# Kernel tuning notes

Hardware: AMD Instinct MI355X
Metric: run time of the kernel (lower is better)

## Reference

```python
import jax, jax.numpy as jnp
import numpy as np

N_NODES = 100000
N_EDGES = 1600000
F_IN = 35
F_OUT = 5
K = 3
HID = 100


def setup_inputs() -> dict:
    key = jax.random.key(0)
    ks = jax.random.split(key, 20)
    p = lambda k, shape: (jax.random.normal(k, shape, dtype=jnp.float32) * 0.1)
    inp = {
        "x": jax.random.normal(ks[0], (N_NODES, F_IN), dtype=jnp.float32),
        "edge_index": jax.random.randint(ks[1], (2, N_EDGES), 0, N_NODES, dtype=jnp.int64),
        "edge_weight": jax.random.uniform(ks[2], (N_EDGES,), dtype=jnp.float32),
        # MLP warm-start: Linear(35,100) -> ReLU -> Linear(100,5)
        "W1": p(ks[3], (F_IN, HID)), "b1": p(ks[4], (HID,)),
        "W2": p(ks[5], (HID, F_OUT)), "b2": p(ks[6], (F_OUT,)),
        # DCRNN gates: DConv weights [2 directions, K, in+out, out]
        "Wz": p(ks[7], (2, K, F_IN + F_OUT, F_OUT)), "bz": p(ks[8], (F_OUT,)),
        "Wr": p(ks[9], (2, K, F_IN + F_OUT, F_OUT)), "br": p(ks[10], (F_OUT,)),
        "Wh": p(ks[11], (2, K, F_IN + F_OUT, F_OUT)), "bh": p(ks[12], (F_OUT,)),
        # head Linear(5,1)
        "Wl": p(ks[13], (F_OUT, 1)), "bl": p(ks[14], (1,)),
    }
    return inp


def reference(x, edge_index, edge_weight, W1, b1, W2, b2, Wz, bz, Wr, br, Wh, bh, Wl, bl):
    n = x.shape[0]
    src, dst = edge_index[0], edge_index[1]
    eps = jnp.asarray(1e-12, x.dtype)
    # random-walk normalization: forward (out-degree) and backward (in-degree) diffusion
    deg_out = jax.ops.segment_sum(edge_weight, src, num_segments=n)
    deg_in = jax.ops.segment_sum(edge_weight, dst, num_segments=n)
    w_fwd = edge_weight / jnp.maximum(deg_out[src], eps)  # [E]
    w_bwd = edge_weight / jnp.maximum(deg_in[dst], eps)   # [E]

    def prop_fwd(X):  # aggregate src -> dst
        return jax.ops.segment_sum(X[src] * w_fwd[:, None], dst, num_segments=n)

    def prop_bwd(X):  # aggregate dst -> src (reversed edges)
        return jax.ops.segment_sum(X[dst] * w_bwd[:, None], src, num_segments=n)

    def dconv(X, W, b):  # W: [2, K, Cin, Cout]
        k_steps = W.shape[1]
        out = X @ W[0, 0] + X @ W[1, 0]
        if k_steps > 1:
            Tf0, Tb0 = X, X
            Tf1, Tb1 = prop_fwd(X), prop_bwd(X)
            out = out + Tf1 @ W[0, 1] + Tb1 @ W[1, 1]
            for k in range(2, k_steps):
                Tf2 = 2.0 * prop_fwd(Tf1) - Tf0
                Tb2 = 2.0 * prop_bwd(Tb1) - Tb0
                out = out + Tf2 @ W[0, k] + Tb2 @ W[1, k]
                Tf0, Tf1 = Tf1, Tf2
                Tb0, Tb1 = Tb1, Tb2
        return out + b

    # MLP warm-start hidden state
    h1 = jax.nn.relu(x @ W1 + b1) @ W2 + b2  # [N, F_OUT]

    # DCRNN GRU cell
    XH = jnp.concatenate([x, h1], axis=1)           # [N, F_IN+F_OUT]
    Z = jax.nn.sigmoid(dconv(XH, Wz, bz))
    R = jax.nn.sigmoid(dconv(XH, Wr, br))
    XHr = jnp.concatenate([x, h1 * R], axis=1)
    H_tilde = jnp.tanh(dconv(XHr, Wh, bh))
    H = Z * h1 + (1.0 - Z) * H_tilde                # [N, F_OUT]

    y = jax.nn.relu(H) @ Wl + bl                    # [N, 1]
    A = w_fwd                                        # normalized adjacency weights [E]
    return y, A
```

## Files before the change

### kernel.cpp

```cpp
#include <hip/hip_runtime.h>
#include <hip/hip_fp16.h>

#define F_IN 35
#define F_OUT 5
#define HID 100
#define BSH 8
#define BMSK 255
#define MAXB 512

__device__ __forceinline__ unsigned qenc(float w) {
  unsigned b = __float_as_uint(w);
  int e = 127 - (int)((b >> 23) & 0xFF);
  unsigned m = (b >> 12) & 0x7FFu;
  if (e < 0) { e = 0; m = 0; }
  if (e > 15) { e = 15; m = 0; }
  return ((unsigned)e << 11) | m;
}
__device__ __forceinline__ float qdec(unsigned q) {
  return __uint_as_float(((127u - (q >> 11)) << 23) | ((q & 0x7FFu) << 12));
}

__device__ __forceinline__ float2 uph2(unsigned u) {
  __half2 h = *reinterpret_cast<const __half2*>(&u);
  return __half22float2(h);
}
__device__ __forceinline__ unsigned pkh2(float a, float b) {
  __half2 h = __floats2half2_rn(a, b);
  return *reinterpret_cast<const unsigned*>(&h);
}

__device__ __forceinline__ int ntli(const int* p) {
  return __builtin_nontemporal_load(p);
}
__device__ __forceinline__ float ntlf(const float* p) {
  return __builtin_nontemporal_load(p);
}
__device__ __forceinline__ void ntsf(float* p, float v) {
  __builtin_nontemporal_store(v, p);
}

__global__ __launch_bounds__(256) void prep_weights(
    const float* __restrict__ Wz, const float* __restrict__ Wr,
    const float* __restrict__ Wh,
    float* __restrict__ WpackA, float* __restrict__ WpackC) {
  int t = blockIdx.x * blockDim.x + threadIdx.x;
  if (t < 40 * 50) {
    int i = t / 50, c = t % 50;
    auto W = [&](const float* Wp, int d, int k, int o) {
      return Wp[((d * 3 + k) * 40 + i) * 5 + o];
    };
    float v;
    if (c < 5)       v = W(Wz,0,0,c)    + W(Wz,1,0,c)    - W(Wz,0,2,c)    - W(Wz,1,2,c);
    else if (c < 10) v = W(Wr,0,0,c-5)  + W(Wr,1,0,c-5)  - W(Wr,0,2,c-5)  - W(Wr,1,2,c-5);
    else if (c < 15) v = W(Wz,0,1,c-10);
    else if (c < 20) v = W(Wr,0,1,c-15);
    else if (c < 25) v = W(Wz,0,2,c-20);
    else if (c < 30) v = W(Wr,0,2,c-25);
    else if (c < 35) v = W(Wz,1,1,c-30);
    else if (c < 40) v = W(Wr,1,1,c-35);
    else if (c < 45) v = W(Wz,1,2,c-40);
    else             v = W(Wr,1,2,c-45);
    WpackA[i * 50 + c] = v;
  }
  if (t < 40 * 25) {
    int i = t / 25, c = t % 25;
    auto W = [&](const float* Wp, int d, int k, int o) {
      return Wp[((d * 3 + k) * 40 + i) * 5 + o];
    };
    float v;
    if (c < 5)       v = W(Wh,0,0,c)    + W(Wh,1,0,c)    - W(Wh,0,2,c)    - W(Wh,1,2,c);
    else if (c < 10) v = W(Wh,0,1,c-5);
    else if (c < 15) v = W(Wh,0,2,c-10);
    else if (c < 20) v = W(Wh,1,1,c-15);
    else             v = W(Wh,1,2,c-20);
    WpackC[i * 25 + c] = v;
  }
}

__global__ __launch_bounds__(256) void hist_kernel(
    const int* __restrict__ ei, int* __restrict__ bcnt_f,
    int* __restrict__ bcnt_b, int E) {
  __shared__ int h[2 * MAXB];
  for (int j = threadIdx.x; j < 2 * MAXB; j += blockDim.x) h[j] = 0;
  __syncthreads();
  for (int e = blockIdx.x * blockDim.x + threadIdx.x; e < E;
       e += gridDim.x * blockDim.x) {
    int s = ntli(ei + e), d = ntli(ei + E + e);
    atomicAdd(&h[d >> BSH], 1);
    atomicAdd(&h[MAXB + (s >> BSH)], 1);
  }
  __syncthreads();
  for (int j = threadIdx.x; j < 2 * MAXB; j += blockDim.x) {
    int v = h[j];
    if (v) {
      if (j < MAXB) atomicAdd(&bcnt_f[j], v);
      else          atomicAdd(&bcnt_b[j - MAXB], v);
    }
  }
}

__global__ __launch_bounds__(512) void scanb_kernel(
    const int* __restrict__ bcnt_f, const int* __restrict__ bcnt_b,
    int* __restrict__ bbase_f, int* __restrict__ bbase_b,
    int* __restrict__ bcur_f, int* __restrict__ bcur_b,
    int* __restrict__ rs_f, int* __restrict__ rs_b,
    int nbuck, int N, int E) {
  __shared__ int s0[MAXB], s1[MAXB];
  int t = threadIdx.x;
  s0[t] = (t < nbuck) ? bcnt_f[t] : 0;
  s1[t] = (t < nbuck) ? bcnt_b[t] : 0;
  __syncthreads();
  for (int off = 1; off < MAXB; off <<= 1) {
    int a = (t >= off) ? s0[t - off] : 0;
    int b = (t >= off) ? s1[t - off] : 0;
    __syncthreads();
    s0[t] += a; s1[t] += b;
    __syncthreads();
  }
  bbase_f[t + 1] = s0[t];
  bbase_b[t + 1] = s1[t];
  bcur_f[t] = t ? s0[t - 1] : 0;
  bcur_b[t] = t ? s1[t - 1] : 0;
  if (t == 0) { bbase_f[0] = 0; bbase_b[0] = 0; rs_f[N] = E; rs_b[N] = E; }
}

__global__ __launch_bounds__(1024) void passB_kernel(
    const int* __restrict__ ei, const float* __restrict__ w,
    int* __restrict__ bcur_f, int* __restrict__ bcur_b,
    int* __restrict__ bid_f, int* __restrict__ bid_b,
    unsigned short* __restrict__ bq_f, unsigned short* __restrict__ bq_b,
    int E) {
  __shared__ int hh[MAXB], cc[MAXB];
  int dir = blockIdx.y;
  int tid = threadIdx.x;
  for (int j = tid; j < MAXB; j += blockDim.x) { hh[j] = 0; cc[j] = 0; }
  __syncthreads();
  size_t c0 = (size_t)blockIdx.x * E / gridDim.x;
  size_t c1 = (size_t)(blockIdx.x + 1) * E / gridDim.x;
  const int* keyc = dir ? ei : ei + E;
  const int* othc = dir ? ei + E : ei;
  int* bcur = dir ? bcur_b : bcur_f;
  int* bid  = dir ? bid_b  : bid_f;
  unsigned short* bq = dir ? bq_b : bq_f;
  for (size_t e = c0 + tid; e < c1; e += blockDim.x) {
    int key = ntli(keyc + e);
    atomicAdd(&hh[key >> BSH], 1);
  }
  __syncthreads();
  for (int j = tid; j < MAXB; j += blockDim.x) {
    int v = hh[j];
    if (v) hh[j] = atomicAdd(&bcur[j], v);
  }
  __syncthreads();
  for (size_t e = c0 + tid; e < c1; e += blockDim.x) {
    int key = ntli(keyc + e);
    int oth = ntli(othc + e);
    unsigned q = qenc(ntlf(w + e));
    int b = key >> BSH;
    int p = hh[b] + atomicAdd(&cc[b], 1);
    bid[p] = oth | ((key & BMSK) << 17);
    bq[p] = (unsigned short)q;
  }
}

__global__ __launch_bounds__(256) void passC_kernel(
    const int* __restrict__ bid_f, const int* __restrict__ bid_b,
    const unsigned short* __restrict__ bq_f,
    const unsigned short* __restrict__ bq_b,
    const int* __restrict__ bbase_f, const int* __restrict__ bbase_b,
    int* __restrict__ adj_f, int* __restrict__ adj_b,
    int* __restrict__ rs_f, int* __restrict__ rs_b,
    float* __restrict__ inv_in, float* __restrict__ inv_out, int N) {
  int dir = blockIdx.y;
  const int* bid = dir ? bid_b : bid_f;
  const unsigned short* bq = dir ? bq_b : bq_f;
  const int* bbase   = dir ? bbase_b  : bbase_f;
  int* adj           = dir ? adj_b    : adj_f;
  int* rs            = dir ? rs_b     : rs_f;
  float* inv         = dir ? inv_out  : inv_in;
  int b = blockIdx.x;
  int base = bbase[b], end = bbase[b + 1];
  __shared__ int cnt[256]; __shared__ float wsum[256];
  __shared__ int loc[256]; __shared__ int cur[256];
  int tid = threadIdx.x;
  cnt[tid] = 0; wsum[tid] = 0.f; cur[tid] = 0;
  __syncthreads();
  for (int i = base + tid; i < end; i += 256) {
    int idv = bid[i];
    int nl = (idv >> 17) & BMSK;
    atomicAdd(&cnt[nl], 1);
    atomicAdd(&wsum[nl], qdec(bq[i]));
  }
  __syncthreads();
  int v = cnt[tid];
  loc[tid] = v;
  __syncthreads();
  for (int off = 1; off < 256; off <<= 1) {
    int a = (tid >= off) ? loc[tid - off] : 0;
    __syncthreads();
    loc[tid] += a;
    __syncthreads();
  }
  int excl = loc[tid] - v;
  int node = (b << BSH) + tid;
  if (node < N) {
    rs[node] = base + excl;
    inv[node] = 1.f / fmaxf(wsum[tid], 1e-12f);
  }
  __syncthreads();
  loc[tid] = excl;
  __syncthreads();
  for (int i = base + tid; i < end; i += 256) {
    int idv = bid[i];
    unsigned q = bq[i];
    int nl = (idv >> 17) & BMSK;
    int p = base + loc[nl] + atomicAdd(&cur[nl], 1);
    adj[p] = (idv & 0x1FFFF) | (int)(q << 17);
  }
}

__global__ __launch_bounds__(256) void wfout_kernel(
    const int* __restrict__ ei, const float* __restrict__ ew,
    const float* __restrict__ inv_out, float* __restrict__ wf, int E) {
  for (int e = blockIdx.x * blockDim.x + threadIdx.x; e < E;
       e += gridDim.x * blockDim.x)
    ntsf(wf + e, ntlf(ew + e) * inv_out[ntli(ei + e)]);
}

__global__ __launch_bounds__(256) void nodeA_kernel(
    const float* __restrict__ x,
    const float* __restrict__ W1, const float* __restrict__ b1,
    const float* __restrict__ W2, const float* __restrict__ b2,
    const float* __restrict__ bz, const float* __restrict__ br,
    const float* __restrict__ WpackA, const float* __restrict__ WpackC,
    const float* __restrict__ inv_out, const float* __restrict__ inv_in,
    float* __restrict__ h1, float* __restrict__ accDz,
    float* __restrict__ accDr, __half* __restrict__ PA_f,
    __half* __restrict__ PA_b, __half* __restrict__ accCx, int N) {
  __shared__ float part[4][64][5];
  int tid = threadIdx.x;
  int lane = tid & 63;
  int q = __builtin_amdgcn_readfirstlane(tid >> 6);
  int n = blockIdx.x * 64 + lane;
  bool act = n < N;
  float xv[40];
  const float* xr = x + (size_t)n * F_IN;
  #pragma unroll
  for (int i = 0; i < F_IN; i++) xv[i] = act ? xr[i] : 0.f;

  float h5[5] = {0.f, 0.f, 0.f, 0.f, 0.f};
  int hbase = q * 25;
  for (int k = 0; k < 25; k++) {
    int hh = hbase + k;
    float a = b1[hh];
    #pragma unroll
    for (int i = 0; i < F_IN; i++) a = fmaf(xv[i], W1[i * HID + hh], a);
    a = fmaxf(a, 0.f);
    #pragma unroll
    for (int o = 0; o < 5; o++) h5[o] = fmaf(a, W2[hh * 5 + o], h5[o]);
  }
  #pragma unroll
  for (int o = 0; o < 5; o++) part[q][lane][o] = h5[o];
  __syncthreads();
  #pragma unroll
  for (int o = 0; o < 5; o++) {
    h5[o] = part[0][lane][o] + part[1][lane][o] + part[2][lane][o] +
            part[3][lane][o] + b2[o];
    xv[F_IN + o] = h5[o];
  }
  if (!act) return;
  if (q == 0) {
    #pragma unroll
    for (int o = 0; o < 5; o++) h1[(size_t)n * 5 + o] = h5[o];
  }
  float sOut = inv_out[n], sIn = inv_in[n];
  int c0 = q * 19, c1 = min(c0 + 19, 75);
  for (int c = c0; c < c1; c++) {
    float a = 0.f;
    if (c < 50) {
      #pragma unroll
      for (int i = 0; i < 40; i++) a = fmaf(xv[i], WpackA[i * 50 + c], a);
    } else {
      #pragma unroll
      for (int i = 0; i < F_IN; i++) a = fmaf(xv[i], WpackC[i * 25 + (c - 50)], a);
    }
    if (c < 5)       accDz[(size_t)n * 5 + c] = a + bz[c];
    else if (c < 10) accDr[(size_t)n * 5 + (c - 5)] = a + br[c - 5];
    else if (c < 30) PA_f[(size_t)n * 20 + (c - 10)] = __float2half(a * sOut);
    else if (c < 50) PA_b[(size_t)n * 20 + (c - 30)] = __float2half(a * sIn);
    else             accCx[(size_t)n * 25 + (c - 50)] = __float2half(a);
  }
}

__global__ __launch_bounds__(256) void p1_kernel(
    const int* __restrict__ rs_f, const int* __restrict__ rs_b,
    const int* __restrict__ adj_f, const int* __restrict__ adj_b,
    const __half* __restrict__ PA_f, const __half* __restrict__ PA_b,
    const float* __restrict__ inv_out, const float* __restrict__ inv_in,
    float* __restrict__ Q1_f, float* __restrict__ Q1_b,
    __half* __restrict__ Q2_f, __half* __restrict__ Q2_b, int N) {
  int dir = blockIdx.x & 1;
  int idx = (blockIdx.x >> 1) * 256 + threadIdx.x;
  if (idx >= 2 * N) return;
  int n = idx >> 1, half = idx & 1;
  const int* rs  = dir ? rs_b : rs_f;
  const int* adj = dir ? adj_b : adj_f;
  const __half* PA = dir ? PA_b : PA_f;
  int i0 = rs[n], i1 = rs[n + 1];
  float acc[10];
  #pragma unroll
  for (int c = 0; c < 10; c++) acc[c] = 0.f;
  int i = i0;
  for (; i + 4 <= i1; i += 4) {
    int a0 = ntli(adj + i),     a1 = ntli(adj + i + 1),
        a2 = ntli(adj + i + 2), a3 = ntli(adj + i + 3);
    const unsigned* r0 = (const unsigned*)(PA + (size_t)(a0 & 0x1FFFF) * 20) + half * 5;
    const unsigned* r1 = (const unsigned*)(PA + (size_t)(a1 & 0x1FFFF) * 20) + half * 5;
    const unsigned* r2 = (const unsigned*)(PA + (size_t)(a2 & 0x1FFFF) * 20) + half * 5;
    const unsigned* r3 = (const unsigned*)(PA + (size_t)(a3 & 0x1FFFF) * 20) + half * 5;
    unsigned u0[5], u1[5], u2[5], u3[5];
    #pragma unroll
    for (int k = 0; k < 5; k++) u0[k] = r0[k];
    #pragma unroll
    for (int k = 0; k < 5; k++) u1[k] = r1[k];
    #pragma unroll
    for (int k = 0; k < 5; k++) u2[k] = r2[k];
    #pragma unroll
    for (int k = 0; k < 5; k++) u3[k] = r3[k];
    float w0 = qdec(((unsigned)a0) >> 17), w1 = qdec(((unsigned)a1) >> 17),
          w2 = qdec(((unsigned)a2) >> 17), w3 = qdec(((unsigned)a3) >> 17);
    #pragma unroll
    for (int k = 0; k < 5; k++) {
      float2 f0 = uph2(u0[k]), f1 = uph2(u1[k]), f2 = uph2(u2[k]), f3 = uph2(u3[k]);
      acc[2*k]   = fmaf(w0, f0.x, acc[2*k]);   acc[2*k+1] = fmaf(w0, f0.y, acc[2*k+1]);
      acc[2*k]   = fmaf(w1, f1.x, acc[2*k]);   acc[2*k+1] = fmaf(w1, f1.y, acc[2*k+1]);
      acc[2*k]   = fmaf(w2, f2.x, acc[2*k]);   acc[2*k+1] = fmaf(w2, f2.y, acc[2*k+1]);
      acc[2*k]   = fmaf(w3, f3.x, acc[2*k]);   acc[2*k+1] = fmaf(w3, f3.y, acc[2*k+1]);
    }
  }
  for (; i < i1; i++) {
    int a = ntli(adj + i);
    float w = qdec(((unsigned)a) >> 17);
    const unsigned* row = (const unsigned*)(PA + (size_t)(a & 0x1FFFF) * 20) + half * 5;
    #pragma unroll
    for (int k = 0; k < 5; k++) {
      float2 f = uph2(row[k]);
      acc[2*k] = fmaf(w, f.x, acc[2*k]); acc[2*k+1] = fmaf(w, f.y, acc[2*k+1]);
    }
  }
  if (!half) {
    float* q = (dir ? Q1_b : Q1_f) + (size_t)n * 10;
    #pragma unroll
    for (int c = 0; c < 10; c++) q[c] = acc[c];
  } else {
    float sc = dir ? inv_in[n] : inv_out[n];
    unsigned* q = (unsigned*)((dir ? Q2_b : Q2_f) + (size_t)n * 12);
    q[0] = pkh2(acc[0] * sc, acc[1] * sc);
    q[1] = pkh2(acc[2] * sc, acc[3] * sc);
    q[2] = pkh2(acc[4] * sc, 0.f);
    q[3] = pkh2(acc[5] * sc, acc[6] * sc);
    q[4] = pkh2(acc[7] * sc, acc[8] * sc);
    q[5] = pkh2(acc[9] * sc, 0.f);
  }
}

__global__ __launch_bounds__(256) void p2a_kernel(
    const int* __restrict__ rs_f, const int* __restrict__ rs_b,
    const int* __restrict__ adj_f, const int* __restrict__ adj_b,
    const __half* __restrict__ Q2_f, const __half* __restrict__ Q2_b,
    float* __restrict__ G_f, float* __restrict__ G_b, int N) {
  int dir = blockIdx.x & 1;
  int idx = (blockIdx.x >> 1) * 256 + threadIdx.x;
  if (idx >= 2 * N) return;
  int n = idx >> 1, grp = idx & 1;
  const int* rs  = dir ? rs_b : rs_f;
  const int* adj = dir ? adj_b : adj_f;
  const __half* Q2 = dir ? Q2_b : Q2_f;
  int i0 = rs[n], i1 = rs[n + 1];
  float a[5];
  #pragma unroll
  for (int c = 0; c < 5; c++) a[c] = 0.f;
  int i = i0;
  for (; i + 8 <= i1; i += 8) {
    int e[8];
    #pragma unroll
    for (int k = 0; k < 8; k++) e[k] = ntli(adj + i + k);
    unsigned u[8][3];
    #pragma unroll
    for (int k = 0; k < 8; k++) {
      const unsigned* row =
          (const unsigned*)(Q2 + (size_t)(e[k] & 0x1FFFF) * 12) + grp * 3;
      u[k][0] = row[0]; u[k][1] = row[1]; u[k][2] = row[2];
    }
    #pragma unroll
    for (int k = 0; k < 8; k++) {
      float w = qdec(((unsigned)e[k]) >> 17);
      float2 f0 = uph2(u[k][0]), f1 = uph2(u[k][1]), f2 = uph2(u[k][2]);
      a[0] = fmaf(w, f0.x, a[0]); a[1] = fmaf(w, f0.y, a[1]);
      a[2] = fmaf(w, f1.x, a[2]); a[3] = fmaf(w, f1.y, a[3]);
      a[4] = fmaf(w, f2.x, a[4]);
    }
  }
  for (; i < i1; i++) {
    int e = ntli(adj + i);
    float w = qdec(((unsigned)e) >> 17);
    const unsigned* row =
        (const unsigned*)(Q2 + (size_t)(e & 0x1FFFF) * 12) + grp * 3;
    float2 f0 = uph2(row[0]), f1 = uph2(row[1]), f2 = uph2(row[2]);
    a[0] = fmaf(w, f0.x, a[0]); a[1] = fmaf(w, f0.y, a[1]);
    a[2] = fmaf(w, f1.x, a[2]); a[3] = fmaf(w, f1.y, a[3]);
    a[4] = fmaf(w, f2.x, a[4]);
  }
  float* g = (dir ? G_b : G_f) + (size_t)n * 10 + grp * 5;
  #pragma unroll
  for (int c = 0; c < 5; c++) g[c] = a[c];
}

__global__ __launch_bounds__(256) void p2b_kernel(
    const float* __restrict__ G_f, const float* __restrict__ G_b,
    const float* __restrict__ Q1_f, const float* __restrict__ Q1_b,
    const float* __restrict__ accDz, const float* __restrict__ accDr,
    const __half* __restrict__ accCx, const float* __restrict__ h1,
    const float* __restrict__ bh, const float* __restrict__ WpackC,
    const float* __restrict__ inv_out, const float* __restrict__ inv_in,
    float* __restrict__ Zg, float* __restrict__ accDh,
    __half* __restrict__ PH_f, __half* __restrict__ PH_b, int N) {
  int t = blockIdx.x * blockDim.x + threadIdx.x;
  int n = t >> 1, l = t & 1;
  if (n >= N) return;
  float r[5], zv[5];
  #pragma unroll
  for (int o = 0; o < 5; o++) {
    float zA = G_f[(size_t)n * 10 + o] + G_b[(size_t)n * 10 + o];
    float rA = G_f[(size_t)n * 10 + 5 + o] + G_b[(size_t)n * 10 + 5 + o];
    float zp = accDz[(size_t)n * 5 + o] + Q1_f[(size_t)n * 10 + o] +
               Q1_b[(size_t)n * 10 + o] + 2.f * zA;
    float rp = accDr[(size_t)n * 5 + o] + Q1_f[(size_t)n * 10 + 5 + o] +
               Q1_b[(size_t)n * 10 + 5 + o] + 2.f * rA;
    zv[o] = 1.f / (1.f + __expf(-zp));
    r[o]  = 1.f / (1.f + __expf(-rp));
  }
  if (l == 0) {
    #pragma unroll
    for (int o = 0; o < 5; o++) Zg[(size_t)n * 5 + o] = zv[o];
  }
  float hr[5];
  #pragma unroll
  for (int o = 0; o < 5; o++) hr[o] = h1[(size_t)n * 5 + o] * r[o];

  float sOut = inv_out[n], sIn = inv_in[n];
  int c0 = l ? 13 : 0, c1 = l ? 25 : 13;
  for (int c = c0; c < c1; c++) {
    float acc = __half2float(accCx[(size_t)n * 25 + c]);
    #pragma unroll
    for (int o = 0; o < 5; o++) acc = fmaf(hr[o], WpackC[(F_IN + o) * 25 + c], acc);
    if (c < 5)       accDh[(size_t)n * 5 + c] = acc + bh[c];
    else if (c < 10) PH_f[(size_t)n * 12 + (c - 5)] = __float2half(acc * sOut);
    else if (c < 15) PH_f[(size_t)n * 12 + 6 + (c - 10)] = __float2half(acc * sOut);
    else if (c < 20) PH_b[(size_t)n * 12 + (c - 15)] = __float2half(acc * sIn);
    else             PH_b[(size_t)n * 12 + 6 + (c - 20)] = __float2half(acc * sIn);
  }
}

__global__ __launch_bounds__(256) void p3_kernel(
    const int* __restrict__ rs_f, const int* __restrict__ rs_b,
    const int* __restrict__ adj_f, const int* __restrict__ adj_b,
    const __half* __restrict__ PH_f, const __half* __restrict__ PH_b,
    const float* __restrict__ inv_out, const float* __restrict__ inv_in,
    float* __restrict__ Q1h_f, float* __restrict__ Q1h_b,
    __half* __restrict__ Q2h_f, __half* __restrict__ Q2h_b, int N) {
  int dir = blockIdx.x & 1;
  int idx = (blockIdx.x >> 1) * 256 + threadIdx.x;
  if (idx >= 2 * N) return;
  int n = idx >> 1, half = idx & 1;
  const int* rs  = dir ? rs_b : rs_f;
  const int* adj = dir ? adj_b : adj_f;
  const __half* PH = dir ? PH_b : PH_f;
  int i0 = rs[n], i1 = rs[n + 1];
  float acc[5];
  #pragma unroll
  for (int c = 0; c < 5; c++) acc[c] = 0.f;
  int i = i0;
  for (; i + 8 <= i1; i += 8) {
    int e[8];
    #pragma unroll
    for (int k = 0; k < 8; k++) e[k] = ntli(adj + i + k);
    unsigned u[8][3];
    #pragma unroll
    for (int k = 0; k < 8; k++) {
      const unsigned* row =
          (const unsigned*)(PH + (size_t)(e[k] & 0x1FFFF) * 12) + half * 3;
      u[k][0] = row[0]; u[k][1] = row[1]; u[k][2] = row[2];
    }
    #pragma unroll
    for (int k = 0; k < 8; k++) {
      float w = qdec(((unsigned)e[k]) >> 17);
      float2 f0 = uph2(u[k][0]), f1 = uph2(u[k][1]), f2 = uph2(u[k][2]);
      acc[0] = fmaf(w, f0.x, acc[0]); acc[1] = fmaf(w, f0.y, acc[1]);
      acc[2] = fmaf(w, f1.x, acc[2]); acc[3] = fmaf(w, f1.y, acc[3]);
      acc[4] = fmaf(w, f2.x, acc[4]);
    }
  }
  for (; i < i1; i++) {
    int a = ntli(adj + i);
    float w = qdec(((unsigned)a) >> 17);
    const unsigned* row =
        (const unsigned*)(PH + (size_t)(a & 0x1FFFF) * 12) + half * 3;
    float2 f0 = uph2(row[0]), f1 = uph2(row[1]), f2 = uph2(row[2]);
    acc[0] = fmaf(w, f0.x, acc[0]); acc[1] = fmaf(w, f0.y, acc[1]);
    acc[2] = fmaf(w, f1.x, acc[2]); acc[3] = fmaf(w, f1.y, acc[3]);
    acc[4] = fmaf(w, f2.x, acc[4]);
  }
  if (!half) {
    float* q = (dir ? Q1h_b : Q1h_f) + (size_t)n * 5;
    #pragma unroll
    for (int c = 0; c < 5; c++) q[c] = acc[c];
  } else {
    float sc = dir ? inv_in[n] : inv_out[n];
    unsigned* q = (unsigned*)((dir ? Q2h_b : Q2h_f) + (size_t)n * 8);
    q[0] = pkh2(acc[0] * sc, acc[1] * sc);
    q[1] = pkh2(acc[2] * sc, acc[3] * sc);
    q[2] = pkh2(acc[4] * sc, 0.f);
  }
}

__global__ __launch_bounds__(256) void p4_kernel(
    const int* __restrict__ rs_f, const int* __restrict__ rs_b,
    const int* __restrict__ adj_f, const int* __restrict__ adj_b,
    const __half* __restrict__ Q2h_f, const __half* __restrict__ Q2h_b,
    const float* __restrict__ Q1h_f, const float* __restrict__ Q1h_b,
    const float* __restrict__ accDh, const float* __restrict__ Zg,
    const float* __restrict__ h1, const float* __restrict__ Wl,
    const float* __restrict__ bl, float* __restrict__ y, int N) {
  int t = blockIdx.x * blockDim.x + threadIdx.x;
  int n = t >> 1, l = t & 1;
  if (n >= N) return;
  const int* rs  = l ? rs_b : rs_f;
  const int* adj = l ? adj_b : adj_f;
  const __half* Q2h = l ? Q2h_b : Q2h_f;
  float a[5];
  #pragma unroll
  for (int c = 0; c < 5; c++) a[c] = 0.f;
  int i0 = rs[n], i1 = rs[n + 1];
  int i = i0;
  for (; i + 8 <= i1; i += 8) {
    int e[8];
    #pragma unroll
    for (int k = 0; k < 8; k++) e[k] = ntli(adj + i + k);
    unsigned u[8][3];
    #pragma unroll
    for (int k = 0; k < 8; k++) {
      const unsigned* row = (const unsigned*)(Q2h + (size_t)(e[k] & 0x1FFFF) * 8);
      u[k][0] = row[0]; u[k][1] = row[1]; u[k][2] = row[2];
    }
    #pragma unroll
    for (int k = 0; k < 8; k++) {
      float w = qdec(((unsigned)e[k]) >> 17);
      float2 f0 = uph2(u[k][0]), f1 = uph2(u[k][1]), f2 = uph2(u[k][2]);
      a[0] = fmaf(w, f0.x, a[0]); a[1] = fmaf(w, f0.y, a[1]);
      a[2] = fmaf(w, f1.x, a[2]); a[3] = fmaf(w, f1.y, a[3]);
      a[4] = fmaf(w, f2.x, a[4]);
    }
  }
  for (; i < i1; i++) {
    int e = ntli(adj + i);
    float w = qdec(((unsigned)e) >> 17);
    const unsigned* row = (const unsigned*)(Q2h + (size_t)(e & 0x1FFFF) * 8);
    float2 f0 = uph2(row[0]), f1 = uph2(row[1]), f2 = uph2(row[2]);
    a[0] = fmaf(w, f0.x, a[0]); a[1] = fmaf(w, f0.y, a[1]);
    a[2] = fmaf(w, f1.x, a[2]); a[3] = fmaf(w, f1.y, a[3]);
    a[4] = fmaf(w, f2.x, a[4]);
  }
  #pragma unroll
  for (int c = 0; c < 5; c++) a[c] += __shfl_xor(a[c], 1);
  if (l) return;
  float acc = bl[0];
  #pragma unroll
  for (int o = 0; o < 5; o++) {
    float pre = accDh[(size_t)n * 5 + o] + Q1h_f[(size_t)n * 5 + o] +
                Q1h_b[(size_t)n * 5 + o] + 2.f * a[o];
    float ht = tanhf(pre);
    float z = Zg[(size_t)n * 5 + o];
    float H = z * h1[(size_t)n * 5 + o] + (1.f - z) * ht;
    acc += fmaxf(H, 0.f) * Wl[o];
  }
  y[n] = acc;
}

extern "C" void kernel_launch(void* const* d_in, const int* in_sizes, int n_in,
                              void* d_out, int out_size, void* d_ws, size_t ws_size,
                              hipStream_t stream) {
  const float* x  = (const float*)d_in[0];
  const int*   ei = (const int*)d_in[1];
  const float* ew = (const float*)d_in[2];
  const float* W1 = (const float*)d_in[3];
  const float* b1 = (const float*)d_in[4];
  const float* W2 = (const float*)d_in[5];
  const float* b2 = (const float*)d_in[6];
  const float* Wz = (const float*)d_in[7];
  const float* bz = (const float*)d_in[8];
  const float* Wr = (const float*)d_in[9];
  const float* br = (const float*)d_in[10];
  const float* Wh = (const float*)d_in[11];
  const float* bh = (const float*)d_in[12];
  const float* Wl = (const float*)d_in[13];
  const float* bl = (const float*)d_in[14];

  const int N = in_sizes[0] / F_IN;
  const int E = in_sizes[2];
  const int nbuck = ((N - 1) >> BSH) + 1;

  float* out = (float*)d_out;
  float* y_out  = out;
  float* wf_out = out + N;

  float* W = (float*)d_ws;
  size_t o = 0;
  int* bcnt_f  = (int*)(W + o); o += MAXB;
  int* bcnt_b  = (int*)(W + o); o += MAXB;
  int* bbase_f = (int*)(W + o); o += MAXB + 2;
  int* bbase_b = (int*)(W + o); o += MAXB + 2;
  int* bcur_f  = (int*)(W + o); o += MAXB;
  int* bcur_b  = (int*)(W + o); o += MAXB;
  int* rs_f    = (int*)(W + o); o += (size_t)N + 1;
  int* rs_b    = (int*)(W + o); o += (size_t)N + 1;
  float* inv_out = W + o; o += N;
  float* inv_in  = W + o; o += N;
  int* adj_f   = (int*)(W + o); o += (size_t)E;
  int* adj_b   = (int*)(W + o); o += (size_t)E;
  float* h1    = W + o; o += (size_t)5 * N;
  float* accDz = W + o; o += (size_t)5 * N;
  float* accDr = W + o; o += (size_t)5 * N;
  float* accDh = W + o; o += (size_t)5 * N;
  float* Zg    = W + o; o += (size_t)5 * N;
  __half* accCx = (__half*)(W + o); o += (size_t)13 * N;
  o = (o + 1) & ~(size_t)1;
  size_t prop0 = o;
  __half* PA_f = (__half*)(W + o); o += (size_t)10 * N;
  __half* PA_b = (__half*)(W + o); o += (size_t)10 * N;
  float* Q1_f  = W + o; o += (size_t)10 * N;
  float* Q1_b  = W + o; o += (size_t)10 * N;
  __half* Q2_f = (__half*)(W + o); o += (size_t)6 * N;
  __half* Q2_b = (__half*)(W + o); o += (size_t)6 * N;
  __half* PH_f = (__half*)(W + o); o += (size_t)6 * N;
  __half* PH_b = (__half*)(W + o); o += (size_t)6 * N;
  float* Q1h_f = W + o; o += (size_t)5 * N;
  float* Q1h_b = W + o; o += (size_t)5 * N;
  o = (o + 1) & ~(size_t)1;
  __half* Q2h_f = (__half*)(W + o); o += (size_t)4 * N;
  __half* Q2h_b = (__half*)(W + o); o += (size_t)4 * N;
  float* G_f   = W + o; o += (size_t)10 * N;
  float* G_b   = W + o; o += (size_t)10 * N;
  float* WpackA = W + o; o += 2000;
  float* WpackC = W + o; o += 1000;

  int* bid_f = (int*)(W + prop0);
  int* bid_b = bid_f + E;
  unsigned short* bq_f = (unsigned short*)(bid_b + E);
  unsigned short* bq_b = bq_f + E;

  const int NB2 = (2 * N + 255) / 256;
  const int NBd = 2 * ((2 * N + 255) / 256);
  const int NBn = (N + 63) / 64;

  prep_weights<<<8, 256, 0, stream>>>(Wz, Wr, Wh, WpackA, WpackC);

  hipMemsetAsync(bcnt_f, 0, 2 * MAXB * sizeof(int), stream);
  hist_kernel<<<512, 256, 0, stream>>>(ei, bcnt_f, bcnt_b, E);
  scanb_kernel<<<1, MAXB, 0, stream>>>(bcnt_f, bcnt_b, bbase_f, bbase_b,
                                       bcur_f, bcur_b, rs_f, rs_b,
                                       nbuck, N, E);
  passB_kernel<<<dim3(128, 2), 1024, 0, stream>>>(ei, ew, bcur_f, bcur_b,
                                                  bid_f, bid_b, bq_f, bq_b, E);
  passC_kernel<<<dim3(nbuck, 2), 256, 0, stream>>>(
      bid_f, bid_b, bq_f, bq_b, bbase_f, bbase_b, adj_f, adj_b,
      rs_f, rs_b, inv_in, inv_out, N);
  wfout_kernel<<<1024, 256, 0, stream>>>(ei, ew, inv_out, wf_out, E);

  nodeA_kernel<<<NBn, 256, 0, stream>>>(x, W1, b1, W2, b2, bz, br, WpackA,
                                        WpackC, inv_out, inv_in,
                                        h1, accDz, accDr, PA_f, PA_b,
                                        accCx, N);

  p1_kernel<<<NBd, 256, 0, stream>>>(rs_f, rs_b, adj_f, adj_b, PA_f, PA_b,
                                     inv_out, inv_in, Q1_f, Q1_b, Q2_f, Q2_b, N);
  p2a_kernel<<<NBd, 256, 0, stream>>>(rs_f, rs_b, adj_f, adj_b, Q2_f, Q2_b,
                                      G_f, G_b, N);
  p2b_kernel<<<NB2, 256, 0, stream>>>(G_f, G_b, Q1_f, Q1_b, accDz, accDr,
                                      accCx, h1, bh, WpackC, inv_out, inv_in,
                                      Zg, accDh, PH_f, PH_b, N);
  p3_kernel<<<NBd, 256, 0, stream>>>(rs_f, rs_b, adj_f, adj_b, PH_f, PH_b,
                                     inv_out, inv_in, Q1h_f, Q1h_b,
                                     Q2h_f, Q2h_b, N);
  p4_kernel<<<NB2, 256, 0, stream>>>(rs_f, rs_b, adj_f, adj_b, Q2h_f, Q2h_b,
                                     Q1h_f, Q1h_b, accDh, Zg, h1, Wl, bl,
                                     y_out, N);
}
```

Before: 410.7 us.

## Replace global histogram pass with per-block local bucket sort and offset matrix

Drops the separate global histogram kernel and memset. Each passB block now sorts its own edge chunk into buckets locally, writes the per-bucket offsets into a small matrix, and stages packed int2 records within its chunk. A scan kernel sums the per-block counts to get bucket bases. passC then gathers each bucket's segments from every block chunk, one wave per chunk, instead of reading one contiguous bucket range. This removes one full read of the edge index and the global atomics, at the cost of scattered segment reads in passC and a serial 128-iteration loop in the scan.

```diff
diff --git a/kernel.cpp b/kernel.cpp
--- a/kernel.cpp
+++ b/kernel.cpp
@@ -7,6 +7,7 @@
 #define BSH 8
 #define BMSK 255
 #define MAXB 512
+#define NBLK 128
 
 __device__ __forceinline__ unsigned qenc(float w) {
   unsigned b = __float_as_uint(w);
@@ -33,6 +34,9 @@
   return __builtin_nontemporal_load(p);
 }
 __device__ __forceinline__ float ntlf(const float* p) {
+  return __builtin_nontemporal_load(p);
+}
+__device__ __forceinline__ long long ntll(const long long* p) {
   return __builtin_nontemporal_load(p);
 }
 __device__ __forceinline__ void ntsf(float* p, float v) {
@@ -77,38 +81,69 @@
   }
 }
 
-__global__ __launch_bounds__(256) void hist_kernel(
-    const int* __restrict__ ei, int* __restrict__ bcnt_f,
-    int* __restrict__ bcnt_b, int E) {
-  __shared__ int h[2 * MAXB];
-  for (int j = threadIdx.x; j < 2 * MAXB; j += blockDim.x) h[j] = 0;
-  __syncthreads();
-  for (int e = blockIdx.x * blockDim.x + threadIdx.x; e < E;
-       e += gridDim.x * blockDim.x) {
-    int s = ntli(ei + e), d = ntli(ei + E + e);
-    atomicAdd(&h[d >> BSH], 1);
-    atomicAdd(&h[MAXB + (s >> BSH)], 1);
-  }
-  __syncthreads();
-  for (int j = threadIdx.x; j < 2 * MAXB; j += blockDim.x) {
-    int v = h[j];
-    if (v) {
-      if (j < MAXB) atomicAdd(&bcnt_f[j], v);
-      else          atomicAdd(&bcnt_b[j - MAXB], v);
-    }
-  }
-}
-
-__global__ __launch_bounds__(512) void scanb_kernel(
-    const int* __restrict__ bcnt_f, const int* __restrict__ bcnt_b,
+__global__ __launch_bounds__(1024) void passB_kernel(
+    const int* __restrict__ ei, const float* __restrict__ w,
+    int2* __restrict__ staged_f, int2* __restrict__ staged_b,
+    int* __restrict__ lomat, int E) {
+  __shared__ int hh[MAXB], sc[MAXB], cc[MAXB];
+  int dir = blockIdx.y;
+  int j = blockIdx.x;
+  int tid = threadIdx.x;
+  for (int k = tid; k < MAXB; k += blockDim.x) { hh[k] = 0; cc[k] = 0; }
+  __syncthreads();
+  size_t c0 = (size_t)j * E / NBLK;
+  size_t c1 = (size_t)(j + 1) * E / NBLK;
+  const int* keyc = dir ? ei : ei + E;
+  const int* othc = dir ? ei + E : ei;
+  int2* staged = dir ? staged_b : staged_f;
+  int* lom = lomat + ((size_t)dir * NBLK + j) * (MAXB + 1);
+  for (size_t e = c0 + tid; e < c1; e += blockDim.x) {
+    int key = ntli(keyc + e);
+    atomicAdd(&hh[key >> BSH], 1);
+  }
+  __syncthreads();
+  if (tid < MAXB) sc[tid] = hh[tid];
+  __syncthreads();
+  for (int off = 1; off < MAXB; off <<= 1) {
+    int a = (tid >= off && tid < MAXB) ? sc[tid - off] : 0;
+    __syncthreads();
+    if (tid < MAXB) sc[tid] += a;
+    __syncthreads();
+  }
+  if (tid < MAXB) {
+    int lo = sc[tid] - hh[tid];
+    lom[tid] = lo;
+    hh[tid] = lo;
+  }
+  if (tid == 0) lom[MAXB] = (int)(c1 - c0);
+  __syncthreads();
+  for (size_t e = c0 + tid; e < c1; e += blockDim.x) {
+    int key = ntli(keyc + e);
+    int oth = ntli(othc + e);
+    unsigned q = qenc(ntlf(w + e));
+    int b = key >> BSH;
+    int p = hh[b] + atomicAdd(&cc[b], 1);
+    staged[c0 + p] = make_int2(oth | ((key & BMSK) << 17), (int)q);
+  }
+}
+
+__global__ __launch_bounds__(512) void scanb2_kernel(
+    const int* __restrict__ lomat,
     int* __restrict__ bbase_f, int* __restrict__ bbase_b,
-    int* __restrict__ bcur_f, int* __restrict__ bcur_b,
     int* __restrict__ rs_f, int* __restrict__ rs_b,
     int nbuck, int N, int E) {
   __shared__ int s0[MAXB], s1[MAXB];
   int t = threadIdx.x;
-  s0[t] = (t < nbuck) ? bcnt_f[t] : 0;
-  s1[t] = (t < nbuck) ? bcnt_b[t] : 0;
+  int cf = 0, cb = 0;
+  if (t < nbuck) {
+    for (int j = 0; j < NBLK; j++) {
+      const int* lf = lomat + (size_t)j * (MAXB + 1);
+      const int* lb = lomat + ((size_t)NBLK + j) * (MAXB + 1);
+      cf += lf[t + 1] - lf[t];
+      cb += lb[t + 1] - lb[t];
+    }
+  }
+  s0[t] = cf; s1[t] = cb;
   __syncthreads();
   for (int off = 1; off < MAXB; off <<= 1) {
     int a = (t >= off) ? s0[t - off] : 0;
@@ -119,77 +154,44 @@
   }
   bbase_f[t + 1] = s0[t];
   bbase_b[t + 1] = s1[t];
-  bcur_f[t] = t ? s0[t - 1] : 0;
-  bcur_b[t] = t ? s1[t - 1] : 0;
   if (t == 0) { bbase_f[0] = 0; bbase_b[0] = 0; rs_f[N] = E; rs_b[N] = E; }
 }
 
-__global__ __launch_bounds__(1024) void passB_kernel(
-    const int* __restrict__ ei, const float* __restrict__ w,
-    int* __restrict__ bcur_f, int* __restrict__ bcur_b,
-    int* __restrict__ bid_f, int* __restrict__ bid_b,
-    unsigned short* __restrict__ bq_f, unsigned short* __restrict__ bq_b,
-    int E) {
-  __shared__ int hh[MAXB], cc[MAXB];
-  int dir = blockIdx.y;
-  int tid = threadIdx.x;
-  for (int j = tid; j < MAXB; j += blockDim.x) { hh[j] = 0; cc[j] = 0; }
-  __syncthreads();
-  size_t c0 = (size_t)blockIdx.x * E / gridDim.x;
-  size_t c1 = (size_t)(blockIdx.x + 1) * E / gridDim.x;
-  const int* keyc = dir ? ei : ei + E;
-  const int* othc = dir ? ei + E : ei;
-  int* bcur = dir ? bcur_b : bcur_f;
-  int* bid  = dir ? bid_b  : bid_f;
-  unsigned short* bq = dir ? bq_b : bq_f;
-  for (size_t e = c0 + tid; e < c1; e += blockDim.x) {
-    int key = ntli(keyc + e);
-    atomicAdd(&hh[key >> BSH], 1);
-  }
-  __syncthreads();
-  for (int j = tid; j < MAXB; j += blockDim.x) {
-    int v = hh[j];
-    if (v) hh[j] = atomicAdd(&bcur[j], v);
-  }
-  __syncthreads();
-  for (size_t e = c0 + tid; e < c1; e += blockDim.x) {
-    int key = ntli(keyc + e);
-    int oth = ntli(othc + e);
-    unsigned q = qenc(ntlf(w + e));
-    int b = key >> BSH;
-    int p = hh[b] + atomicAdd(&cc[b], 1);
-    bid[p] = oth | ((key & BMSK) << 17);
-    bq[p] = (unsigned short)q;
-  }
-}
-
 __global__ __launch_bounds__(256) void passC_kernel(
-    const int* __restrict__ bid_f, const int* __restrict__ bid_b,
-    const unsigned short* __restrict__ bq_f,
-    const unsigned short* __restrict__ bq_b,
+    const int2* __restrict__ staged_f, const int2* __restrict__ staged_b,
+    const int* __restrict__ lomat,
     const int* __restrict__ bbase_f, const int* __restrict__ bbase_b,
     int* __restrict__ adj_f, int* __restrict__ adj_b,
     int* __restrict__ rs_f, int* __restrict__ rs_b,
-    float* __restrict__ inv_in, float* __restrict__ inv_out, int N) {
+    float* __restrict__ inv_in, float* __restrict__ inv_out, int N, int E) {
   int dir = blockIdx.y;
-  const int* bid = dir ? bid_b : bid_f;
-  const unsigned short* bq = dir ? bq_b : bq_f;
-  const int* bbase   = dir ? bbase_b  : bbase_f;
-  int* adj           = dir ? adj_b    : adj_f;
-  int* rs            = dir ? rs_b     : rs_f;
-  float* inv         = dir ? inv_out  : inv_in;
+  const long long* staged =
+      (const long long*)(dir ? staged_b : staged_f);
+  const int* lomd = lomat + (size_t)dir * NBLK * (MAXB + 1);
+  const int* bbase = dir ? bbase_b : bbase_f;
+  int* adj = dir ? adj_b : adj_f;
+  int* rs  = dir ? rs_b : rs_f;
+  float* inv = dir ? inv_out : inv_in;
   int b = blockIdx.x;
-  int base = bbase[b], end = bbase[b + 1];
+  int base = bbase[b];
   __shared__ int cnt[256]; __shared__ float wsum[256];
   __shared__ int loc[256]; __shared__ int cur[256];
   int tid = threadIdx.x;
+  int wave = tid >> 6, lane = tid & 63;
   cnt[tid] = 0; wsum[tid] = 0.f; cur[tid] = 0;
   __syncthreads();
-  for (int i = base + tid; i < end; i += 256) {
-    int idv = bid[i];
-    int nl = (idv >> 17) & BMSK;
-    atomicAdd(&cnt[nl], 1);
-    atomicAdd(&wsum[nl], qdec(bq[i]));
+  for (int j = wave; j < NBLK; j += 4) {
+    size_t cj = (size_t)j * E / NBLK;
+    const int* lj = lomd + (size_t)j * (MAXB + 1);
+    int lo0 = lj[b], lo1 = lj[b + 1];
+    for (int i = lo0 + lane; i < lo1; i += 64) {
+      long long it = ntll(staged + cj + i);
+      int idv = (int)(unsigned)(it & 0xFFFFFFFFll);
+      unsigned q = (unsigned)((unsigned long long)it >> 32);
+      int nl = (idv >> 17) & BMSK;
+      atomicAdd(&cnt[nl], 1);
+      atomicAdd(&wsum[nl], qdec(q));
+    }
   }
   __syncthreads();
   int v = cnt[tid];
@@ -210,12 +212,18 @@
   __syncthreads();
   loc[tid] = excl;
   __syncthreads();
-  for (int i = base + tid; i < end; i += 256) {
-    int idv = bid[i];
-    unsigned q = bq[i];
-    int nl = (idv >> 17) & BMSK;
-    int p = base + loc[nl] + atomicAdd(&cur[nl], 1);
-    adj[p] = (idv & 0x1FFFF) | (int)(q << 17);
+  for (int j = wave; j < NBLK; j += 4) {
+    size_t cj = (size_t)j * E / NBLK;
+    const int* lj = lomd + (size_t)j * (MAXB + 1);
+    int lo0 = lj[b], lo1 = lj[b + 1];
+    for (int i = lo0 + lane; i < lo1; i += 64) {
+      long long it = ntll(staged + cj + i);
+      int idv = (int)(unsigned)(it & 0xFFFFFFFFll);
+      int q = (int)((unsigned long long)it >> 32);
+      int nl = (idv >> 17) & BMSK;
+      int p = base + loc[nl] + atomicAdd(&cur[nl], 1);
+      adj[p] = (idv & 0x1FFFF) | (q << 17);
+    }
   }
 }
 
@@ -616,12 +624,9 @@
 
   float* W = (float*)d_ws;
   size_t o = 0;
-  int* bcnt_f  = (int*)(W + o); o += MAXB;
-  int* bcnt_b  = (int*)(W + o); o += MAXB;
   int* bbase_f = (int*)(W + o); o += MAXB + 2;
   int* bbase_b = (int*)(W + o); o += MAXB + 2;
-  int* bcur_f  = (int*)(W + o); o += MAXB;
-  int* bcur_b  = (int*)(W + o); o += MAXB;
+  int* lomat   = (int*)(W + o); o += (size_t)2 * NBLK * (MAXB + 1);
   int* rs_f    = (int*)(W + o); o += (size_t)N + 1;
   int* rs_b    = (int*)(W + o); o += (size_t)N + 1;
   float* inv_out = W + o; o += N;
@@ -654,10 +659,8 @@
   float* WpackA = W + o; o += 2000;
   float* WpackC = W + o; o += 1000;
 
-  int* bid_f = (int*)(W + prop0);
-  int* bid_b = bid_f + E;
-  unsigned short* bq_f = (unsigned short*)(bid_b + E);
-  unsigned short* bq_b = bq_f + E;
+  int2* staged_f = (int2*)(W + prop0);
+  int2* staged_b = staged_f + E;
 
   const int NB2 = (2 * N + 255) / 256;
   const int NBd = 2 * ((2 * N + 255) / 256);
@@ -665,16 +668,13 @@
 
   prep_weights<<<8, 256, 0, stream>>>(Wz, Wr, Wh, WpackA, WpackC);
 
-  hipMemsetAsync(bcnt_f, 0, 2 * MAXB * sizeof(int), stream);
-  hist_kernel<<<512, 256, 0, stream>>>(ei, bcnt_f, bcnt_b, E);
-  scanb_kernel<<<1, MAXB, 0, stream>>>(bcnt_f, bcnt_b, bbase_f, bbase_b,
-                                       bcur_f, bcur_b, rs_f, rs_b,
-                                       nbuck, N, E);
-  passB_kernel<<<dim3(128, 2), 1024, 0, stream>>>(ei, ew, bcur_f, bcur_b,
-                                                  bid_f, bid_b, bq_f, bq_b, E);
+  passB_kernel<<<dim3(NBLK, 2), 1024, 0, stream>>>(ei, ew, staged_f, staged_b,
+                                                   lomat, E);
+  scanb2_kernel<<<1, MAXB, 0, stream>>>(lomat, bbase_f, bbase_b,
+                                        rs_f, rs_b, nbuck, N, E);
   passC_kernel<<<dim3(nbuck, 2), 256, 0, stream>>>(
-      bid_f, bid_b, bq_f, bq_b, bbase_f, bbase_b, adj_f, adj_b,
-      rs_f, rs_b, inv_in, inv_out, N);
+      staged_f, staged_b, lomat, bbase_f, bbase_b, adj_f, adj_b,
+      rs_f, rs_b, inv_in, inv_out, N, E);
   wfout_kernel<<<1024, 256, 0, stream>>>(ei, ew, inv_out, wf_out, E);
 
   nodeA_kernel<<<NBn, 256, 0, stream>>>(x, W1, b1, W2, b2, bz, br, WpackA,
```

After: 397.1 us. 3.3% less time.
